# Performance work log

Hardware: AMD Instinct MI355X
Metric: run time of the kernel (lower is better)

Reference implementation:

```python
import jax, jax.numpy as jnp
import numpy as np

B, S, H, E = 32, 2048, 1024, 1024
NEG = -10000000000.0


def setup_inputs() -> dict:
    key = jax.random.key(0)
    ks = jax.random.split(key, 8)
    scale = 1.0 / np.sqrt(H)
    return {
        "hidden": jax.random.normal(ks[0], (B, H), jnp.float32),
        "encoder_outputs": jax.random.normal(ks[1], (B, S, E), jnp.float32),
        "mask": jax.random.randint(ks[2], (B, S), 0, 2, jnp.int32),
        "W_h": jax.random.normal(ks[3], (H, H), jnp.float32) * scale,
        "b_h": jax.random.normal(ks[4], (H,), jnp.float32) * scale,
        "W_e": jax.random.normal(ks[5], (E, H), jnp.float32) * scale,
        "b_e": jax.random.normal(ks[6], (H,), jnp.float32) * scale,
        "v": jax.random.normal(ks[7], (H,), jnp.float32) * scale,
    }


def reference(hidden, encoder_outputs, mask, W_h, b_h, W_e, b_e, v):
    # hidden proj: (B,H) -> (B,1,H); encoder proj: (B,S,E) -> (B,S,H)
    h_proj = (hidden @ W_h + b_h)[:, None, :]
    e_proj = jnp.einsum("bse,eh->bsh", encoder_outputs, W_e) + b_e
    energy = jnp.tanh(h_proj + e_proj)                      # (B,S,H)
    attention = jnp.einsum("bsh,h->bs", energy, v)          # (B,S)
    attention = jnp.where(mask == 0, NEG, attention)
    attention_weights = jax.nn.softmax(attention, axis=1)   # (B,S)
    context = jnp.einsum("bs,bse->be", attention_weights, encoder_outputs)
    return (context, attention_weights)
```

## Files before the change

### kernel.cpp

```cpp
#include <hip/hip_runtime.h>

#define NEGV -10000000000.0f

typedef _Float16 half8 __attribute__((ext_vector_type(8)));
typedef float f32x4 __attribute__((ext_vector_type(4)));

__device__ __forceinline__ void gld16(const void* g, void* l) {
  __builtin_amdgcn_global_load_lds((const __attribute__((address_space(1))) void*)g,
                                   (__attribute__((address_space(3))) void*)l,
                                   16, 0, 0);
}

__device__ __forceinline__ float fast_tanh(float x) {
  const float e = __expf(2.0f * x);
  return 1.0f - 2.0f * __builtin_amdgcn_rcpf(e + 1.0f);
}

__global__ __launch_bounds__(256) void prep_kernel(
    const float* __restrict__ enc, _Float16* __restrict__ enc16,
    const float* __restrict__ We, _Float16* __restrict__ W16T,
    const float* __restrict__ hidden, const float* __restrict__ W_h,
    const float* __restrict__ b_h, const float* __restrict__ b_e,
    float* __restrict__ hpb) {
  __shared__ float tile[32][33];
  const int bid = blockIdx.x;
  const int tid = threadIdx.x;

  if (bid < 128) {
    const int b = bid >> 2;
    const int h = ((bid & 3) << 8) | tid;
    const float* hb = hidden + b * 1024;
    float a0 = 0.f, a1 = 0.f, a2 = 0.f, a3 = 0.f;
    #pragma unroll 4
    for (int k = 0; k < 1024; k += 4) {
      a0 = fmaf(hb[k + 0], W_h[(size_t)(k + 0) * 1024 + h], a0);
      a1 = fmaf(hb[k + 1], W_h[(size_t)(k + 1) * 1024 + h], a1);
      a2 = fmaf(hb[k + 2], W_h[(size_t)(k + 2) * 1024 + h], a2);
      a3 = fmaf(hb[k + 3], W_h[(size_t)(k + 3) * 1024 + h], a3);
    }
    hpb[b * 1024 + h] = b_h[h] + b_e[h] + ((a0 + a1) + (a2 + a3));
  } else if (bid < 128 + 1024) {
    const int tb = bid - 128;
    const int n0 = (tb & 31) << 5, k0 = (tb >> 5) << 5;
    const int tx = tid & 31, ty = tid >> 5;
    #pragma unroll
    for (int i = 0; i < 4; ++i) {
      const int r = ty + (i << 3);
      tile[r][tx] = We[(size_t)(k0 + r) * 1024 + n0 + tx];
    }
    __syncthreads();
    #pragma unroll
    for (int i = 0; i < 4; ++i) {
      const int r = ty + (i << 3);
      W16T[(size_t)(n0 + r) * 1024 + k0 + tx] = (_Float16)tile[tx][r];
    }
  } else {
    const size_t base = ((size_t)(bid - 1152) * 256 + tid) * 8;
    const float4 x = *(const float4*)(enc + base);
    const float4 y = *(const float4*)(enc + base + 4);
    half8 h;
    h[0] = (_Float16)x.x; h[1] = (_Float16)x.y; h[2] = (_Float16)x.z; h[3] = (_Float16)x.w;
    h[4] = (_Float16)y.x; h[5] = (_Float16)y.y; h[6] = (_Float16)y.z; h[7] = (_Float16)y.w;
    *(half8*)(enc16 + base) = h;
  }
}

__global__ __launch_bounds__(512, 2) void attn_gemm8_kernel(
    const _Float16* __restrict__ enc16, const _Float16* __restrict__ W16T,
    const float* __restrict__ hpb, const float* __restrict__ v,
    const int* __restrict__ mask, float* __restrict__ logits) {
  __shared__ __align__(16) _Float16 Abuf[3][256 * 32];
  __shared__ __align__(16) _Float16 Bbuf[3][256 * 32];
  __shared__ float hp_s[1024];
  __shared__ float vh_s[1024];
  __shared__ float red[1024];

  const int tid = threadIdx.x;
  const int wid = tid >> 6;
  const int lane = tid & 63;
  const int l15 = lane & 15;
  const int qq = lane >> 4;
  const int wr = wid >> 2;
  const int wc = wid & 3;
  const int m0 = blockIdx.x << 8;
  const int b = blockIdx.x >> 3;

  for (int i = tid; i < 1024; i += 512) {
    hp_s[i] = hpb[(b << 10) + i];
    vh_s[i] = v[i];
  }

  const int r0 = tid >> 2;
  const int r1 = r0 + 128;
  const int g0 = tid & 3;
  const int sc = (g0 ^ ((r0 >> 1) & 3)) << 4;
  const int ldsoff0 = (wid << 10);
  const int ldsoff1 = (wid << 10) + 8192;

  const char* encb = (const char*)(enc16 + (size_t)m0 * 1024);
  const char* wb0 = (const char*)W16T;

  auto stageA = [&](int buf, int t) {
    const int colb = ((t & 31) << 6) + sc;
    char* base = (char*)(&Abuf[buf][0]);
    gld16(encb + (size_t)r0 * 2048 + colb, base + ldsoff0);
    gld16(encb + (size_t)r1 * 2048 + colb, base + ldsoff1);
  };
  auto stageB = [&](int buf, int t) {
    const char* wb = wb0 + ((size_t)(t >> 5) << 19);
    const int colb = ((t & 31) << 6) + sc;
    char* base = (char*)(&Bbuf[buf][0]);
    gld16(wb + (size_t)r0 * 2048 + colb, base + ldsoff0);
    gld16(wb + (size_t)r1 * 2048 + colb, base + ldsoff1);
  };

  int aoff[2][4], boff[4];
  #pragma unroll
  for (int mh = 0; mh < 2; ++mh)
    #pragma unroll
    for (int mi = 0; mi < 4; ++mi) {
      const int row = (wr << 7) + (mh << 6) + (mi << 4) + l15;
      aoff[mh][mi] = (row << 6) + ((qq ^ ((row >> 1) & 3)) << 4);
    }
  #pragma unroll
  for (int ni = 0; ni < 4; ++ni) {
    const int np = (wc << 6) + (ni << 4) + l15;
    boff[ni] = (np << 6) + ((qq ^ ((np >> 1) & 3)) << 4);
  }

  f32x4 acc[8][4];
  float rowsum[8][4];
  #pragma unroll
  for (int mi = 0; mi < 8; ++mi)
    #pragma unroll
    for (int j = 0; j < 4; ++j) {
      acc[mi][j] = (f32x4){0.f, 0.f, 0.f, 0.f};
      rowsum[mi][j] = 0.f;
    }

  stageA(0, 0); stageB(0, 0);
  stageA(1, 1); stageB(1, 1);
  __syncthreads();

  int bi = 0;
  #pragma unroll 1
  for (int t = 0; t < 128; ++t) {
    const int bi2 = (bi >= 1) ? bi - 1 : bi + 2;
    const char* A = (const char*)(&Abuf[bi][0]);
    const char* B = (const char*)(&Bbuf[bi][0]);
    half8 a[4], bf[4];

    #pragma unroll
    for (int mi = 0; mi < 4; ++mi) a[mi] = *(const half8*)(A + aoff[0][mi]);
    #pragma unroll
    for (int ni = 0; ni < 4; ++ni) bf[ni] = *(const half8*)(B + boff[ni]);
    if (t < 126) stageA(bi2, t + 2);
    __builtin_amdgcn_s_barrier();
    asm volatile("s_waitcnt lgkmcnt(0)" ::: "memory");
    __builtin_amdgcn_s_setprio(1);
    #pragma unroll
    for (int mi = 0; mi < 4; ++mi)
      #pragma unroll
      for (int ni = 0; ni < 4; ++ni)
        acc[mi][ni] = __builtin_amdgcn_mfma_f32_16x16x32_f16(a[mi], bf[ni], acc[mi][ni], 0, 0, 0);
    __builtin_amdgcn_s_setprio(0);
    __builtin_amdgcn_s_barrier();

    #pragma unroll
    for (int mi = 0; mi < 4; ++mi) a[mi] = *(const half8*)(A + aoff[1][mi]);
    if (t < 126) stageB(bi2, t + 2);
    __builtin_amdgcn_s_barrier();
    asm volatile("s_waitcnt lgkmcnt(0)" ::: "memory");
    __builtin_amdgcn_s_setprio(1);
    #pragma unroll
    for (int mi = 0; mi < 4; ++mi)
      #pragma unroll
      for (int ni = 0; ni < 4; ++ni)
        acc[4 + mi][ni] = __builtin_amdgcn_mfma_f32_16x16x32_f16(a[mi], bf[ni], acc[4 + mi][ni], 0, 0, 0);
    __builtin_amdgcn_s_setprio(0);

    if (t < 126) asm volatile("s_waitcnt vmcnt(4)" ::: "memory");
    else         asm volatile("s_waitcnt vmcnt(0)" ::: "memory");
    __builtin_amdgcn_s_barrier();

    if ((t & 31) == 31) {
      const int nt = t >> 5;
      const int hb = (nt << 8) + (wc << 6);
      #pragma unroll
      for (int ni = 0; ni < 4; ++ni) {
        const int h = hb + (ni << 4) + l15;
        const float hv = hp_s[h];
        const float vv = vh_s[h];
        #pragma unroll
        for (int mi = 0; mi < 8; ++mi) {
          #pragma unroll
          for (int r = 0; r < 4; ++r)
            rowsum[mi][r] += fast_tanh(acc[mi][ni][r] + hv) * vv;
          acc[mi][ni] = (f32x4){0.f, 0.f, 0.f, 0.f};
        }
      }
    }
    bi = (bi >= 2) ? 0 : bi + 1;
  }

  #pragma unroll
  for (int mi = 0; mi < 8; ++mi)
    #pragma unroll
    for (int r = 0; r < 4; ++r) {
      float s = rowsum[mi][r];
      s += __shfl_xor(s, 1);
      s += __shfl_xor(s, 2);
      s += __shfl_xor(s, 4);
      s += __shfl_xor(s, 8);
      rowsum[mi][r] = s;
    }
  __syncthreads();
  if (l15 == 0) {
    #pragma unroll
    for (int mi = 0; mi < 8; ++mi)
      #pragma unroll
      for (int r = 0; r < 4; ++r) {
        const int row = (wr << 7) + (mi << 4) + (qq << 2) + r;
        red[(row << 2) + wc] = rowsum[mi][r];
      }
  }
  __syncthreads();
  if (tid < 256) {
    const float s = red[tid << 2] + red[(tid << 2) + 1] + red[(tid << 2) + 2] + red[(tid << 2) + 3];
    const int m = m0 + tid;
    logits[m] = (mask[(b << 11) + (m & 2047)] == 0) ? NEGV : s;
  }
}

__global__ void softmax_kernel(const float* __restrict__ logits, float* __restrict__ wout) {
  __shared__ float red[4];
  const int b = blockIdx.x, tid = threadIdx.x;
  const int wid = tid >> 6, lane = tid & 63;
  const float* lb = logits + b * 2048;
  float x[8];
  #pragma unroll
  for (int j = 0; j < 8; ++j) x[j] = lb[tid + j * 256];
  float m = x[0];
  #pragma unroll
  for (int j = 1; j < 8; ++j) m = fmaxf(m, x[j]);
  #pragma unroll
  for (int off = 32; off > 0; off >>= 1) m = fmaxf(m, __shfl_xor(m, off));
  if (lane == 0) red[wid] = m;
  __syncthreads();
  m = fmaxf(fmaxf(red[0], red[1]), fmaxf(red[2], red[3]));
  __syncthreads();
  float e[8];
  float s = 0.f;
  #pragma unroll
  for (int j = 0; j < 8; ++j) { e[j] = expf(x[j] - m); s += e[j]; }
  #pragma unroll
  for (int off = 32; off > 0; off >>= 1) s += __shfl_xor(s, off);
  if (lane == 0) red[wid] = s;
  __syncthreads();
  s = red[0] + red[1] + red[2] + red[3];
  const float inv = 1.0f / s;
  #pragma unroll
  for (int j = 0; j < 8; ++j) wout[b * 2048 + tid + j * 256] = e[j] * inv;
}

__global__ void context16_kernel(const _Float16* __restrict__ enc16,
                                 const float* __restrict__ wout, float* __restrict__ ctx) {
  const int b = blockIdx.x >> 4;
  const int ch = blockIdx.x & 15;
  const int tl = threadIdx.x & 127;
  const int sh = threadIdx.x >> 7;
  float a[8] = {0.f, 0.f, 0.f, 0.f, 0.f, 0.f, 0.f, 0.f};
  #pragma unroll 1
  for (int i = 0; i < 64; ++i) {
    const int s = (ch << 7) + (i << 1) + sh;
    const float w = wout[(b << 11) + s];
    const half8 r = *(const half8*)(enc16 + (((size_t)(b << 11) + s) << 10) + (tl << 3));
    #pragma unroll
    for (int j = 0; j < 8; ++j) a[j] = fmaf(w, (float)r[j], a[j]);
  }
  float* c = ctx + (b << 10) + (tl << 3);
  #pragma unroll
  for (int j = 0; j < 8; ++j) atomicAdd(c + j, a[j]);
}

extern "C" void kernel_launch(void* const* d_in, const int* in_sizes, int n_in,
                              void* d_out, int out_size, void* d_ws, size_t ws_size,
                              hipStream_t stream) {
  const float* hidden = (const float*)d_in[0];
  const float* enc    = (const float*)d_in[1];
  const int*   mask   = (const int*)d_in[2];
  const float* W_h    = (const float*)d_in[3];
  const float* b_h    = (const float*)d_in[4];
  const float* W_e    = (const float*)d_in[5];
  const float* b_e    = (const float*)d_in[6];
  const float* v      = (const float*)d_in[7];

  float* ctx  = (float*)d_out;
  float* wout = (float*)d_out + 32 * 1024;

  char* ws = (char*)d_ws;
  const size_t ENC16_BYTES = 134217728ULL;
  _Float16* enc16 = (_Float16*)ws;
  _Float16* W16T  = (_Float16*)(ws + ENC16_BYTES);
  float* hpb      = (float*)(ws + ENC16_BYTES + 2097152);
  float* logits   = (float*)(ws + ENC16_BYTES + 2097152 + 131072);

  hipMemsetAsync(ctx, 0, 32 * 1024 * sizeof(float), stream);
  hipLaunchKernelGGL(prep_kernel, dim3(1152 + 32768), dim3(256), 0, stream,
                     enc, enc16, W_e, W16T, hidden, W_h, b_h, b_e, hpb);
  hipLaunchKernelGGL(attn_gemm8_kernel, dim3(256), dim3(512), 0, stream,
                     enc16, W16T, hpb, v, mask, logits);
  hipLaunchKernelGGL(softmax_kernel, dim3(32), dim3(256), 0, stream, logits, wout);
  hipLaunchKernelGGL(context16_kernel, dim3(512), dim3(256), 0, stream, enc16, wout, ctx);
}
```

Before: 292.1 us.

## Fuse fp32-to-fp16 encoder conversion into first GEMM panel

Removes the separate pass in the prep kernel that converts encoder_outputs to fp16. During the first N-panel (32 K-steps), the GEMM kernel now loads fp32 encoder rows directly, converts them in registers, writes them to swizzled LDS and writes the fp16 copy to global memory for later panels and the context kernel. This saves one full read of the fp32 tensor plus a kernel's worth of conversion traffic. The cost is that the first panel uses a simpler double-buffered register-staged pipeline with more barriers and full vmcnt waits, so it may stall more.

```diff
diff --git a/kernel.cpp b/kernel.cpp
--- a/kernel.cpp
+++ b/kernel.cpp
@@ -17,7 +17,6 @@
 }
 
 __global__ __launch_bounds__(256) void prep_kernel(
-    const float* __restrict__ enc, _Float16* __restrict__ enc16,
     const float* __restrict__ We, _Float16* __restrict__ W16T,
     const float* __restrict__ hidden, const float* __restrict__ W_h,
     const float* __restrict__ b_h, const float* __restrict__ b_e,
@@ -39,7 +38,7 @@
       a3 = fmaf(hb[k + 3], W_h[(size_t)(k + 3) * 1024 + h], a3);
     }
     hpb[b * 1024 + h] = b_h[h] + b_e[h] + ((a0 + a1) + (a2 + a3));
-  } else if (bid < 128 + 1024) {
+  } else {
     const int tb = bid - 128;
     const int n0 = (tb & 31) << 5, k0 = (tb >> 5) << 5;
     const int tx = tid & 31, ty = tid >> 5;
@@ -54,19 +53,12 @@
       const int r = ty + (i << 3);
       W16T[(size_t)(n0 + r) * 1024 + k0 + tx] = (_Float16)tile[tx][r];
     }
-  } else {
-    const size_t base = ((size_t)(bid - 1152) * 256 + tid) * 8;
-    const float4 x = *(const float4*)(enc + base);
-    const float4 y = *(const float4*)(enc + base + 4);
-    half8 h;
-    h[0] = (_Float16)x.x; h[1] = (_Float16)x.y; h[2] = (_Float16)x.z; h[3] = (_Float16)x.w;
-    h[4] = (_Float16)y.x; h[5] = (_Float16)y.y; h[6] = (_Float16)y.z; h[7] = (_Float16)y.w;
-    *(half8*)(enc16 + base) = h;
   }
 }
 
 __global__ __launch_bounds__(512, 2) void attn_gemm8_kernel(
-    const _Float16* __restrict__ enc16, const _Float16* __restrict__ W16T,
+    const float* __restrict__ enc32, _Float16* __restrict__ enc16,
+    const _Float16* __restrict__ W16T,
     const float* __restrict__ hpb, const float* __restrict__ v,
     const int* __restrict__ mask, float* __restrict__ logits) {
   __shared__ __align__(16) _Float16 Abuf[3][256 * 32];
@@ -94,6 +86,7 @@
   const int r1 = r0 + 128;
   const int g0 = tid & 3;
   const int sc = (g0 ^ ((r0 >> 1) & 3)) << 4;
+  const int scE = (g0 ^ ((r0 >> 1) & 3)) << 3;
   const int ldsoff0 = (wid << 10);
   const int ldsoff1 = (wid << 10) + 8192;
 
@@ -114,6 +107,33 @@
     gld16(wb + (size_t)r1 * 2048 + colb, base + ldsoff1);
   };
 
+  f32x4 af[4];
+  half8 bh[2];
+  auto issueP0 = [&](int t) {
+    const float* ap0 = enc32 + (size_t)(m0 + r0) * 1024 + (t << 5) + scE;
+    const float* ap1 = enc32 + (size_t)(m0 + r1) * 1024 + (t << 5) + scE;
+    af[0] = *(const f32x4*)ap0; af[1] = *(const f32x4*)(ap0 + 4);
+    af[2] = *(const f32x4*)ap1; af[3] = *(const f32x4*)(ap1 + 4);
+    bh[0] = *(const half8*)(W16T + (size_t)r0 * 1024 + (t << 5) + scE);
+    bh[1] = *(const half8*)(W16T + (size_t)r1 * 1024 + (t << 5) + scE);
+  };
+  auto writeP0 = [&](int par, int t) {
+    half8 h0, h1;
+    #pragma unroll
+    for (int j = 0; j < 4; ++j) {
+      h0[j] = (_Float16)af[0][j]; h0[4 + j] = (_Float16)af[1][j];
+      h1[j] = (_Float16)af[2][j]; h1[4 + j] = (_Float16)af[3][j];
+    }
+    char* Ab = (char*)(&Abuf[par][0]);
+    char* Bb = (char*)(&Bbuf[par][0]);
+    *(half8*)(Ab + (r0 << 6) + (g0 << 4)) = h0;
+    *(half8*)(Ab + (r1 << 6) + (g0 << 4)) = h1;
+    *(half8*)(Bb + (r0 << 6) + (g0 << 4)) = bh[0];
+    *(half8*)(Bb + (r1 << 6) + (g0 << 4)) = bh[1];
+    *(half8*)(enc16 + (size_t)(m0 + r0) * 1024 + (t << 5) + scE) = h0;
+    *(half8*)(enc16 + (size_t)(m0 + r1) * 1024 + (t << 5) + scE) = h1;
+  };
+
   int aoff[2][4], boff[4];
   #pragma unroll
   for (int mh = 0; mh < 2; ++mh)
@@ -138,13 +158,78 @@
       rowsum[mi][j] = 0.f;
     }
 
-  stageA(0, 0); stageB(0, 0);
-  stageA(1, 1); stageB(1, 1);
+  auto panel_epilogue = [&](int nt) {
+    const int hb = (nt << 8) + (wc << 6);
+    #pragma unroll
+    for (int ni = 0; ni < 4; ++ni) {
+      const int h = hb + (ni << 4) + l15;
+      const float hv = hp_s[h];
+      const float vv = vh_s[h];
+      #pragma unroll
+      for (int mi = 0; mi < 8; ++mi) {
+        #pragma unroll
+        for (int r = 0; r < 4; ++r)
+          rowsum[mi][r] += fast_tanh(acc[mi][ni][r] + hv) * vv;
+        acc[mi][ni] = (f32x4){0.f, 0.f, 0.f, 0.f};
+      }
+    }
+  };
+
+  issueP0(0);
+  asm volatile("s_waitcnt vmcnt(0)" ::: "memory");
+  writeP0(0, 0);
+  asm volatile("s_waitcnt lgkmcnt(0)" ::: "memory");
+  __builtin_amdgcn_s_barrier();
+
+  #pragma unroll 1
+  for (int t = 0; t < 32; ++t) {
+    const int par = t & 1, npar = par ^ 1;
+    const char* A = (const char*)(&Abuf[par][0]);
+    const char* B = (const char*)(&Bbuf[par][0]);
+    half8 a[4], bf[4];
+
+    #pragma unroll
+    for (int mi = 0; mi < 4; ++mi) a[mi] = *(const half8*)(A + aoff[0][mi]);
+    #pragma unroll
+    for (int ni = 0; ni < 4; ++ni) bf[ni] = *(const half8*)(B + boff[ni]);
+    if (t < 31) issueP0(t + 1);
+    __builtin_amdgcn_s_barrier();
+    asm volatile("s_waitcnt lgkmcnt(0)" ::: "memory");
+    __builtin_amdgcn_s_setprio(1);
+    #pragma unroll
+    for (int mi = 0; mi < 4; ++mi)
+      #pragma unroll
+      for (int ni = 0; ni < 4; ++ni)
+        acc[mi][ni] = __builtin_amdgcn_mfma_f32_16x16x32_f16(a[mi], bf[ni], acc[mi][ni], 0, 0, 0);
+    __builtin_amdgcn_s_setprio(0);
+    __builtin_amdgcn_s_barrier();
+
+    #pragma unroll
+    for (int mi = 0; mi < 4; ++mi) a[mi] = *(const half8*)(A + aoff[1][mi]);
+    __builtin_amdgcn_s_barrier();
+    asm volatile("s_waitcnt lgkmcnt(0)" ::: "memory");
+    __builtin_amdgcn_s_setprio(1);
+    #pragma unroll
+    for (int mi = 0; mi < 4; ++mi)
+      #pragma unroll
+      for (int ni = 0; ni < 4; ++ni)
+        acc[4 + mi][ni] = __builtin_amdgcn_mfma_f32_16x16x32_f16(a[mi], bf[ni], acc[4 + mi][ni], 0, 0, 0);
+    __builtin_amdgcn_s_setprio(0);
+
+    asm volatile("s_waitcnt vmcnt(0)" ::: "memory");
+    if (t < 31) writeP0(npar, t + 1);
+    asm volatile("s_waitcnt lgkmcnt(0)" ::: "memory");
+    __builtin_amdgcn_s_barrier();
+  }
+  panel_epilogue(0);
+
+  stageA(0, 32); stageB(0, 32);
+  stageA(1, 33); stageB(1, 33);
   __syncthreads();
 
   int bi = 0;
   #pragma unroll 1
-  for (int t = 0; t < 128; ++t) {
+  for (int t = 32; t < 128; ++t) {
     const int bi2 = (bi >= 1) ? bi - 1 : bi + 2;
     const char* A = (const char*)(&Abuf[bi][0]);
     const char* B = (const char*)(&Bbuf[bi][0]);
@@ -183,23 +268,7 @@
     else         asm volatile("s_waitcnt vmcnt(0)" ::: "memory");
     __builtin_amdgcn_s_barrier();
 
-    if ((t & 31) == 31) {
-      const int nt = t >> 5;
-      const int hb = (nt << 8) + (wc << 6);
-      #pragma unroll
-      for (int ni = 0; ni < 4; ++ni) {
-        const int h = hb + (ni << 4) + l15;
-        const float hv = hp_s[h];
-        const float vv = vh_s[h];
-        #pragma unroll
-        for (int mi = 0; mi < 8; ++mi) {
-          #pragma unroll
-          for (int r = 0; r < 4; ++r)
-            rowsum[mi][r] += fast_tanh(acc[mi][ni][r] + hv) * vv;
-          acc[mi][ni] = (f32x4){0.f, 0.f, 0.f, 0.f};
-        }
-      }
-    }
+    if ((t & 31) == 31) panel_epilogue(t >> 5);
     bi = (bi >= 2) ? 0 : bi + 1;
   }
 
@@ -306,10 +375,10 @@
   float* logits   = (float*)(ws + ENC16_BYTES + 2097152 + 131072);
 
   hipMemsetAsync(ctx, 0, 32 * 1024 * sizeof(float), stream);
-  hipLaunchKernelGGL(prep_kernel, dim3(1152 + 32768), dim3(256), 0, stream,
-                     enc, enc16, W_e, W16T, hidden, W_h, b_h, b_e, hpb);
+  hipLaunchKernelGGL(prep_kernel, dim3(1152), dim3(256), 0, stream,
+                     W_e, W16T, hidden, W_h, b_h, b_e, hpb);
   hipLaunchKernelGGL(attn_gemm8_kernel, dim3(256), dim3(512), 0, stream,
-                     enc16, W16T, hpb, v, mask, logits);
+                     enc, enc16, W16T, hpb, v, mask, logits);
   hipLaunchKernelGGL(softmax_kernel, dim3(32), dim3(256), 0, stream, logits, wout);
   hipLaunchKernelGGL(context16_kernel, dim3(512), dim3(256), 0, stream, enc16, wout, ctx);
 }
```

After: 309.3 us. 1.06x slower.
